# Optimization experiments

Hardware: AMD Instinct MI355X
Metric: run time of the kernel (lower is better)

## Reference

```python
import jax, jax.numpy as jnp
import numpy as np

HIDDEN = 2048
NUM_HEADS = 32
NUM_KV_HEADS = 8
HEAD_DIM = HIDDEN // NUM_HEADS  # 64


def setup_inputs() -> dict:
    key = jax.random.key(0)
    ks = jax.random.split(key, 5)
    s = 0.02
    x = jax.random.normal(ks[0], (2, 2048, HIDDEN), dtype=jnp.float32)
    Wq = jax.random.normal(ks[1], (HIDDEN, NUM_HEADS * HEAD_DIM), dtype=jnp.float32) * s
    Wk = jax.random.normal(ks[2], (HIDDEN, NUM_KV_HEADS * HEAD_DIM), dtype=jnp.float32) * s
    Wv = jax.random.normal(ks[3], (HIDDEN, NUM_KV_HEADS * HEAD_DIM), dtype=jnp.float32) * s
    Wo = jax.random.normal(ks[4], (NUM_HEADS * HEAD_DIM, HIDDEN), dtype=jnp.float32) * s
    return {"x": x, "Wq": Wq, "Wk": Wk, "Wv": Wv, "Wo": Wo}


def reference(x, Wq, Wk, Wv, Wo):
    b, s, _ = x.shape
    # projections: [b, s, h, d] -> [b, h, s, d]
    q = (x @ Wq).reshape(b, s, NUM_HEADS, HEAD_DIM).transpose(0, 2, 1, 3)
    k = (x @ Wk).reshape(b, s, NUM_KV_HEADS, HEAD_DIM).transpose(0, 2, 1, 3)
    v = (x @ Wv).reshape(b, s, NUM_KV_HEADS, HEAD_DIM).transpose(0, 2, 1, 3)
    rep = NUM_HEADS // NUM_KV_HEADS
    # repeat_interleave along head dim (consecutive copies), matching torch
    k = jnp.repeat(k, rep, axis=1)
    v = jnp.repeat(v, rep, axis=1)
    scale = HEAD_DIM ** (-0.5)
    attn = jnp.einsum("bhqd,bhkd->bhqk", q, k) * scale  # [b,h,s,s]
    attn = jax.nn.softmax(attn, axis=-1)
    out = jnp.einsum("bhqk,bhkd->bhqd", attn, v)
    out = out.transpose(0, 2, 1, 3).reshape(b, s, NUM_HEADS * HEAD_DIM)
    return out @ Wo
```

## Files before the change

### kernel.cpp

```cpp
#include <hip/hip_runtime.h>

typedef __attribute__((ext_vector_type(8))) short short8;
typedef __attribute__((ext_vector_type(4))) float f32x4;
typedef __attribute__((ext_vector_type(4))) unsigned short u16x4;
typedef __attribute__((ext_vector_type(8))) unsigned short u16x8;

__device__ __forceinline__ unsigned short f2bf(float f) {
  union { float f; unsigned u; } v; v.f = f;
  unsigned r = v.u + 0x7FFFu + ((v.u >> 16) & 1u);
  return (unsigned short)(r >> 16);
}

#define GLL16(g, l) \
  __builtin_amdgcn_global_load_lds((const __attribute__((address_space(1))) void*)(g), \
                                   (__attribute__((address_space(3))) void*)(l), 16, 0, 0)

__device__ __forceinline__ void tpose_body(const float* __restrict__ in,
                                           unsigned short* __restrict__ out,
                                           int C, int ldo, int c0, int r0,
                                           float (*tile)[33], int tx, int ty) {
#pragma unroll
  for (int i = 0; i < 4; ++i)
    tile[ty + i * 8][tx] = in[(size_t)(r0 + ty + i * 8) * C + c0 + tx];
  __syncthreads();
#pragma unroll
  for (int i = 0; i < 4; ++i)
    out[(size_t)(c0 + ty + i * 8) * ldo + r0 + tx] = f2bf(tile[tx][ty + i * 8]);
}

__global__ __launch_bounds__(256) void prep_kernel(const float* __restrict__ x,
                                                   const float* __restrict__ Wq,
                                                   const float* __restrict__ Wk,
                                                   const float* __restrict__ Wv,
                                                   const float* __restrict__ Wo,
                                                   unsigned short* __restrict__ xb,
                                                   unsigned short* __restrict__ wqkvt,
                                                   unsigned short* __restrict__ wot) {
  __shared__ float tile[32][33];
  const int bid = blockIdx.x;
  if (bid < 4096) {
    const int i = bid * 256 + threadIdx.x;
    const f32x4* p = (const f32x4*)x;
    f32x4 a = p[2 * i], b = p[2 * i + 1];
    u16x8 r;
    r[0] = f2bf(a[0]); r[1] = f2bf(a[1]); r[2] = f2bf(a[2]); r[3] = f2bf(a[3]);
    r[4] = f2bf(b[0]); r[5] = f2bf(b[1]); r[6] = f2bf(b[2]); r[7] = f2bf(b[3]);
    ((u16x8*)xb)[i] = r;
    return;
  }
  const int tx = threadIdx.x & 31, ty = threadIdx.x >> 5;
  int b2 = bid - 4096;
  if (b2 < 4096) {
    tpose_body(Wq, wqkvt, 2048, 2048, (b2 & 63) * 32, (b2 >> 6) * 32, tile, tx, ty);
    return;
  }
  b2 -= 4096;
  if (b2 < 1024) {
    tpose_body(Wk, wqkvt + (size_t)2048 * 2048, 512, 2048, (b2 & 15) * 32, (b2 >> 4) * 32, tile, tx, ty);
    return;
  }
  b2 -= 1024;
  if (b2 < 1024) {
    tpose_body(Wv, wqkvt + (size_t)2560 * 2048, 512, 2048, (b2 & 15) * 32, (b2 >> 4) * 32, tile, tx, ty);
    return;
  }
  b2 -= 1024;
  tpose_body(Wo, wot, 2048, 2048, (b2 & 63) * 32, (b2 >> 6) * 32, tile, tx, ty);
}

__global__ __launch_bounds__(256) void gemm_qkv_kernel(const unsigned short* __restrict__ A,
                                                       const unsigned short* __restrict__ BT,
                                                       unsigned short* __restrict__ Cq,
                                                       unsigned short* __restrict__ VT) {
  __shared__ unsigned short As[2][128 * 32];
  __shared__ unsigned short Bs[2][128 * 32];
  const int tid = threadIdx.x;
  const int wave = tid >> 6, lane = tid & 63;
  const int r16 = lane & 15, g = lane >> 4;
  const int n0 = blockIdx.x * 128, m0 = blockIdx.y * 128;
  const int wr = wave >> 1, wc = wave & 1;
  f32x4 acc[4][4] = {};
  const int so = wave * 1024 + lane * 16;

  auto STAGE = [&](int kt, int bufi) {
    const int k0 = kt * 32;
#pragma unroll
    for (int i = 0; i < 2; ++i) {
      const int o = i * 4096 + so;
      const int row = o >> 6;
      const int ke = (o & 63) >> 1;
      GLL16(A + (size_t)(m0 + row) * 2048 + k0 + ke, (char*)As[bufi] + i * 4096 + wave * 1024);
      GLL16(BT + (size_t)(n0 + row) * 2048 + k0 + ke, (char*)Bs[bufi] + i * 4096 + wave * 1024);
    }
  };
  STAGE(0, 0);
  __syncthreads();
  for (int kt = 0; kt < 64; ++kt) {
    const int cur = kt & 1;
    if (kt < 63) STAGE(kt + 1, cur ^ 1);
    short8 af[4], bfr[4];
#pragma unroll
    for (int mi = 0; mi < 4; ++mi) {
      const int row = wr * 64 + mi * 16 + r16;
      af[mi] = *(const short8*)((const char*)As[cur] + row * 64 + g * 16);
    }
#pragma unroll
    for (int ni = 0; ni < 4; ++ni) {
      const int row = wc * 64 + ni * 16 + r16;
      bfr[ni] = *(const short8*)((const char*)Bs[cur] + row * 64 + g * 16);
    }
#pragma unroll
    for (int mi = 0; mi < 4; ++mi)
#pragma unroll
      for (int ni = 0; ni < 4; ++ni)
        acc[mi][ni] = __builtin_amdgcn_mfma_f32_16x16x32_bf16(af[mi], bfr[ni], acc[mi][ni], 0, 0, 0);
    __syncthreads();
  }
  const float qs = 0.18033688f;
#pragma unroll
  for (int mi = 0; mi < 4; ++mi) {
#pragma unroll
    for (int ni = 0; ni < 4; ++ni) {
      const int n = n0 + wc * 64 + ni * 16 + r16;
      const int mb = m0 + wr * 64 + mi * 16 + g * 4;
      f32x4 v = acc[mi][ni];
      if (n < 2560) {
        const float s = (n < 2048) ? qs : 1.0f;
#pragma unroll
        for (int r = 0; r < 4; ++r) Cq[(size_t)(mb + r) * 3072 + n] = f2bf(v[r] * s);
      } else {
        const int d = n - 2560;
        const int bb = mb >> 11, s0 = mb & 2047;
        const int s0p = (s0 & ~31) | (((s0 >> 2) & 3) << 3) | (((s0 >> 4) & 1) << 2);
        u16x4 pk;
#pragma unroll
        for (int r = 0; r < 4; ++r) pk[r] = f2bf(v[r]);
        *(u16x4*)(VT + (size_t)(bb * 512 + d) * 2048 + s0p) = pk;
      }
    }
  }
}

__global__ __launch_bounds__(256) void gemm_out_kernel(const unsigned short* __restrict__ A,
                                                       const unsigned short* __restrict__ BT,
                                                       float* __restrict__ Co) {
  __shared__ unsigned short As[2][128 * 32];
  __shared__ unsigned short Bs[2][128 * 32];
  const int tid = threadIdx.x;
  const int wave = tid >> 6, lane = tid & 63;
  const int r16 = lane & 15, g = lane >> 4;
  const int n0 = blockIdx.x * 128, m0 = blockIdx.y * 128;
  const int wr = wave >> 1, wc = wave & 1;
  f32x4 acc[4][4] = {};
  const int so = wave * 1024 + lane * 16;

  auto STAGE = [&](int kt, int bufi) {
    const int k0 = kt * 32;
#pragma unroll
    for (int i = 0; i < 2; ++i) {
      const int o = i * 4096 + so;
      const int row = o >> 6;
      const int ke = (o & 63) >> 1;
      GLL16(A + (size_t)(m0 + row) * 2048 + k0 + ke, (char*)As[bufi] + i * 4096 + wave * 1024);
      GLL16(BT + (size_t)(n0 + row) * 2048 + k0 + ke, (char*)Bs[bufi] + i * 4096 + wave * 1024);
    }
  };
  STAGE(0, 0);
  __syncthreads();
  for (int kt = 0; kt < 64; ++kt) {
    const int cur = kt & 1;
    if (kt < 63) STAGE(kt + 1, cur ^ 1);
    short8 af[4], bfr[4];
#pragma unroll
    for (int mi = 0; mi < 4; ++mi) {
      const int row = wr * 64 + mi * 16 + r16;
      af[mi] = *(const short8*)((const char*)As[cur] + row * 64 + g * 16);
    }
#pragma unroll
    for (int ni = 0; ni < 4; ++ni) {
      const int row = wc * 64 + ni * 16 + r16;
      bfr[ni] = *(const short8*)((const char*)Bs[cur] + row * 64 + g * 16);
    }
#pragma unroll
    for (int mi = 0; mi < 4; ++mi)
#pragma unroll
      for (int ni = 0; ni < 4; ++ni)
        acc[mi][ni] = __builtin_amdgcn_mfma_f32_16x16x32_bf16(af[mi], bfr[ni], acc[mi][ni], 0, 0, 0);
    __syncthreads();
  }
#pragma unroll
  for (int mi = 0; mi < 4; ++mi)
#pragma unroll
    for (int ni = 0; ni < 4; ++ni) {
      const int n = n0 + wc * 64 + ni * 16 + r16;
      const int mb = m0 + wr * 64 + mi * 16 + g * 4;
      f32x4 v = acc[mi][ni];
#pragma unroll
      for (int r = 0; r < 4; ++r) Co[(size_t)(mb + r) * 2048 + n] = v[r];
    }
}

__global__ __launch_bounds__(256) void attn_kernel(const unsigned short* __restrict__ QKV,
                                                   const unsigned short* __restrict__ VT,
                                                   unsigned short* __restrict__ O) {
  __shared__ unsigned short Ks[2][64 * 64];
  __shared__ unsigned short Vs[2][64 * 64];
  const int tid = threadIdx.x;
  const int wave = tid >> 6, lane = tid & 63;
  const int r16 = lane & 15, g = lane >> 4;
  const int qt = blockIdx.x, bh = blockIdx.y;
  const int b = bh >> 5, h = bh & 31, kvh = h >> 2;
  const int qtok0 = b * 2048 + qt * 128 + wave * 32;
  short8 qf[2][2];
#pragma unroll
  for (int mt = 0; mt < 2; ++mt)
#pragma unroll
    for (int kh = 0; kh < 2; ++kh)
      qf[mt][kh] = *(const short8*)(QKV + (size_t)(qtok0 + mt * 16 + r16) * 3072 + h * 64 + kh * 32 + g * 8);
  union { unsigned u[4]; short8 s; } ones;
  ones.u[0] = ones.u[1] = ones.u[2] = ones.u[3] = 0x3F803F80u;
  f32x4 oa[2][4] = {};
  f32x4 lacc[2] = {};
  const unsigned short* Kb = QKV + (size_t)b * 2048 * 3072 + 2048 + kvh * 64;
  const unsigned short* Vb = VT + (size_t)(b * 512 + kvh * 64) * 2048;
  const int so = wave * 1024 + lane * 16;

  auto STAGE = [&](int t, int bufi) {
    const int kv0 = t * 64;
#pragma unroll
    for (int i = 0; i < 2; ++i) {
      const int o = i * 4096 + so;
      const int row = o >> 7;
      const int c = ((((o >> 4) & 7) ^ (row & 7))) * 8;
      GLL16(Kb + (size_t)(kv0 + row) * 3072 + c, (char*)Ks[bufi] + i * 4096 + wave * 1024);
      GLL16(Vb + (size_t)row * 2048 + kv0 + c, (char*)Vs[bufi] + i * 4096 + wave * 1024);
    }
  };
  STAGE(0, 0);
  __syncthreads();
  for (int t = 0; t < 32; ++t) {
    const int cur = t & 1;
    if (t < 31) STAGE(t + 1, cur ^ 1);
    f32x4 sc[2][4];
    __builtin_amdgcn_s_setprio(1);
#pragma unroll
    for (int jt = 0; jt < 4; ++jt) {
      short8 kf0, kf1;
      const int j = jt * 16 + r16;
      kf0 = *(const short8*)((const char*)Ks[cur] + j * 128 + ((g * 16) ^ ((j & 7) << 4)));
      kf1 = *(const short8*)((const char*)Ks[cur] + j * 128 + ((64 + g * 16) ^ ((j & 7) << 4)));
#pragma unroll
      for (int mt = 0; mt < 2; ++mt) {
        f32x4 z = {-8.f, -8.f, -8.f, -8.f};
        z = __builtin_amdgcn_mfma_f32_16x16x32_bf16(kf0, qf[mt][0], z, 0, 0, 0);
        z = __builtin_amdgcn_mfma_f32_16x16x32_bf16(kf1, qf[mt][1], z, 0, 0, 0);
        sc[mt][jt] = z;
      }
    }
    __builtin_amdgcn_s_setprio(0);
    short8 pa[2][2];
#pragma unroll
    for (int mt = 0; mt < 2; ++mt) {
      unsigned pk[4][2];
#pragma unroll
      for (int jt = 0; jt < 4; ++jt) {
        float p0 = __builtin_amdgcn_exp2f(sc[mt][jt][0]);
        float p1 = __builtin_amdgcn_exp2f(sc[mt][jt][1]);
        float p2 = __builtin_amdgcn_exp2f(sc[mt][jt][2]);
        float p3 = __builtin_amdgcn_exp2f(sc[mt][jt][3]);
        asm("v_cvt_pk_bf16_f32 %0, %1, %2" : "=v"(pk[jt][0]) : "v"(p0), "v"(p1));
        asm("v_cvt_pk_bf16_f32 %0, %1, %2" : "=v"(pk[jt][1]) : "v"(p2), "v"(p3));
      }
#pragma unroll
      for (int kh = 0; kh < 2; ++kh) {
        union { unsigned u[4]; short8 s; } pu;
        pu.u[0] = pk[2 * kh][0]; pu.u[1] = pk[2 * kh][1];
        pu.u[2] = pk[2 * kh + 1][0]; pu.u[3] = pk[2 * kh + 1][1];
        pa[mt][kh] = pu.s;
      }
    }
    __builtin_amdgcn_s_setprio(1);
#pragma unroll
    for (int mt = 0; mt < 2; ++mt) {
      lacc[mt] = __builtin_amdgcn_mfma_f32_16x16x32_bf16(pa[mt][0], ones.s, lacc[mt], 0, 0, 0);
      lacc[mt] = __builtin_amdgcn_mfma_f32_16x16x32_bf16(pa[mt][1], ones.s, lacc[mt], 0, 0, 0);
    }
#pragma unroll
    for (int dt = 0; dt < 4; ++dt) {
      const int d = dt * 16 + r16;
      const char* vrow = (const char*)Vs[cur] + d * 128;
      const int sw = (d & 7) << 4;
#pragma unroll
      for (int kh = 0; kh < 2; ++kh) {
        short8 vf = *(const short8*)(vrow + ((kh * 64 + g * 16) ^ sw));
#pragma unroll
        for (int mt = 0; mt < 2; ++mt)
          oa[mt][dt] = __builtin_amdgcn_mfma_f32_16x16x32_bf16(pa[mt][kh], vf, oa[mt][dt], 0, 0, 0);
      }
    }
    __builtin_amdgcn_s_setprio(0);
    __syncthreads();
  }
#pragma unroll
  for (int mt = 0; mt < 2; ++mt)
#pragma unroll
    for (int dt = 0; dt < 4; ++dt)
#pragma unroll
      for (int r = 0; r < 4; ++r)
        O[(size_t)(qtok0 + mt * 16 + g * 4 + r) * 2048 + h * 64 + dt * 16 + r16] =
            f2bf(oa[mt][dt][r] / lacc[mt][r]);
}

extern "C" void kernel_launch(void* const* d_in, const int* in_sizes, int n_in,
                              void* d_out, int out_size, void* d_ws, size_t ws_size,
                              hipStream_t stream) {
  const float* x  = (const float*)d_in[0];
  const float* Wq = (const float*)d_in[1];
  const float* Wk = (const float*)d_in[2];
  const float* Wv = (const float*)d_in[3];
  const float* Wo = (const float*)d_in[4];
  char* w = (char*)d_ws;
  unsigned short* xb    = (unsigned short*)(w);
  unsigned short* wqkvt = (unsigned short*)(w + 16777216);
  unsigned short* wot   = (unsigned short*)(w + 29360128);
  unsigned short* qkv   = (unsigned short*)(w + 37748736);
  unsigned short* vt    = (unsigned short*)(w + 62914560);
  unsigned short* ob    = (unsigned short*)(w + 67108864);
  float* out = (float*)d_out;

  prep_kernel<<<14336, 256, 0, stream>>>(x, Wq, Wk, Wv, Wo, xb, wqkvt, wot);
  gemm_qkv_kernel<<<dim3(24, 32), 256, 0, stream>>>(xb, wqkvt, qkv, vt);
  attn_kernel<<<dim3(16, 64), 256, 0, stream>>>(qkv, vt, ob);
  gemm_out_kernel<<<dim3(16, 32), 256, 0, stream>>>(ob, wot, out);
}
```

Before: 236.5 us.

## Split attention block into 8 waves of 16 query rows each

The attention kernel now launches 512 threads per block, and each of 8 waves handles 16 query rows instead of 32. The K/V staging is spread so each thread issues one global-to-LDS load per tile instead of two. This aims to raise wave-level parallelism and latency hiding per block while cutting per-wave registers. In exchange, each K/V fragment read from LDS now feeds only one query tile, so LDS read traffic per MFMA doubles, and the larger block synchronises more waves at each barrier.

```diff
diff --git a/kernel.cpp b/kernel.cpp
--- a/kernel.cpp
+++ b/kernel.cpp
@@ -200,7 +200,7 @@
     }
 }
 
-__global__ __launch_bounds__(256) void attn_kernel(const unsigned short* __restrict__ QKV,
+__global__ __launch_bounds__(512) void attn_kernel(const unsigned short* __restrict__ QKV,
                                                    const unsigned short* __restrict__ VT,
                                                    unsigned short* __restrict__ O) {
   __shared__ unsigned short Ks[2][64 * 64];
@@ -210,64 +210,53 @@
   const int r16 = lane & 15, g = lane >> 4;
   const int qt = blockIdx.x, bh = blockIdx.y;
   const int b = bh >> 5, h = bh & 31, kvh = h >> 2;
-  const int qtok0 = b * 2048 + qt * 128 + wave * 32;
-  short8 qf[2][2];
-#pragma unroll
-  for (int mt = 0; mt < 2; ++mt)
-#pragma unroll
-    for (int kh = 0; kh < 2; ++kh)
-      qf[mt][kh] = *(const short8*)(QKV + (size_t)(qtok0 + mt * 16 + r16) * 3072 + h * 64 + kh * 32 + g * 8);
+  const int qtok0 = b * 2048 + qt * 128 + wave * 16;
+  short8 qf[2];
+#pragma unroll
+  for (int kh = 0; kh < 2; ++kh)
+    qf[kh] = *(const short8*)(QKV + (size_t)(qtok0 + r16) * 3072 + h * 64 + kh * 32 + g * 8);
   union { unsigned u[4]; short8 s; } ones;
   ones.u[0] = ones.u[1] = ones.u[2] = ones.u[3] = 0x3F803F80u;
-  f32x4 oa[2][4] = {};
-  f32x4 lacc[2] = {};
+  f32x4 oa[4] = {};
+  f32x4 lacc = {};
   const unsigned short* Kb = QKV + (size_t)b * 2048 * 3072 + 2048 + kvh * 64;
   const unsigned short* Vb = VT + (size_t)(b * 512 + kvh * 64) * 2048;
   const int so = wave * 1024 + lane * 16;
 
   auto STAGE = [&](int t, int bufi) {
     const int kv0 = t * 64;
-#pragma unroll
-    for (int i = 0; i < 2; ++i) {
-      const int o = i * 4096 + so;
-      const int row = o >> 7;
-      const int c = ((((o >> 4) & 7) ^ (row & 7))) * 8;
-      GLL16(Kb + (size_t)(kv0 + row) * 3072 + c, (char*)Ks[bufi] + i * 4096 + wave * 1024);
-      GLL16(Vb + (size_t)row * 2048 + kv0 + c, (char*)Vs[bufi] + i * 4096 + wave * 1024);
-    }
+    const int row = so >> 7;
+    const int c = ((((so >> 4) & 7) ^ (row & 7))) * 8;
+    GLL16(Kb + (size_t)(kv0 + row) * 3072 + c, (char*)Ks[bufi] + wave * 1024);
+    GLL16(Vb + (size_t)row * 2048 + kv0 + c, (char*)Vs[bufi] + wave * 1024);
   };
   STAGE(0, 0);
   __syncthreads();
   for (int t = 0; t < 32; ++t) {
     const int cur = t & 1;
     if (t < 31) STAGE(t + 1, cur ^ 1);
-    f32x4 sc[2][4];
+    f32x4 sc[4];
     __builtin_amdgcn_s_setprio(1);
 #pragma unroll
     for (int jt = 0; jt < 4; ++jt) {
-      short8 kf0, kf1;
       const int j = jt * 16 + r16;
-      kf0 = *(const short8*)((const char*)Ks[cur] + j * 128 + ((g * 16) ^ ((j & 7) << 4)));
-      kf1 = *(const short8*)((const char*)Ks[cur] + j * 128 + ((64 + g * 16) ^ ((j & 7) << 4)));
-#pragma unroll
-      for (int mt = 0; mt < 2; ++mt) {
-        f32x4 z = {-8.f, -8.f, -8.f, -8.f};
-        z = __builtin_amdgcn_mfma_f32_16x16x32_bf16(kf0, qf[mt][0], z, 0, 0, 0);
-        z = __builtin_amdgcn_mfma_f32_16x16x32_bf16(kf1, qf[mt][1], z, 0, 0, 0);
-        sc[mt][jt] = z;
-      }
+      short8 kf0 = *(const short8*)((const char*)Ks[cur] + j * 128 + ((g * 16) ^ ((j & 7) << 4)));
+      short8 kf1 = *(const short8*)((const char*)Ks[cur] + j * 128 + ((64 + g * 16) ^ ((j & 7) << 4)));
+      f32x4 z = {-8.f, -8.f, -8.f, -8.f};
+      z = __builtin_amdgcn_mfma_f32_16x16x32_bf16(kf0, qf[0], z, 0, 0, 0);
+      z = __builtin_amdgcn_mfma_f32_16x16x32_bf16(kf1, qf[1], z, 0, 0, 0);
+      sc[jt] = z;
     }
     __builtin_amdgcn_s_setprio(0);
-    short8 pa[2][2];
-#pragma unroll
-    for (int mt = 0; mt < 2; ++mt) {
+    short8 pa[2];
+    {
       unsigned pk[4][2];
 #pragma unroll
       for (int jt = 0; jt < 4; ++jt) {
-        float p0 = __builtin_amdgcn_exp2f(sc[mt][jt][0]);
-        float p1 = __builtin_amdgcn_exp2f(sc[mt][jt][1]);
-        float p2 = __builtin_amdgcn_exp2f(sc[mt][jt][2]);
-        float p3 = __builtin_amdgcn_exp2f(sc[mt][jt][3]);
+        float p0 = __builtin_amdgcn_exp2f(sc[jt][0]);
+        float p1 = __builtin_amdgcn_exp2f(sc[jt][1]);
+        float p2 = __builtin_amdgcn_exp2f(sc[jt][2]);
+        float p3 = __builtin_amdgcn_exp2f(sc[jt][3]);
         asm("v_cvt_pk_bf16_f32 %0, %1, %2" : "=v"(pk[jt][0]) : "v"(p0), "v"(p1));
         asm("v_cvt_pk_bf16_f32 %0, %1, %2" : "=v"(pk[jt][1]) : "v"(p2), "v"(p3));
       }
@@ -276,15 +265,12 @@
         union { unsigned u[4]; short8 s; } pu;
         pu.u[0] = pk[2 * kh][0]; pu.u[1] = pk[2 * kh][1];
         pu.u[2] = pk[2 * kh + 1][0]; pu.u[3] = pk[2 * kh + 1][1];
-        pa[mt][kh] = pu.s;
+        pa[kh] = pu.s;
       }
     }
     __builtin_amdgcn_s_setprio(1);
-#pragma unroll
-    for (int mt = 0; mt < 2; ++mt) {
-      lacc[mt] = __builtin_amdgcn_mfma_f32_16x16x32_bf16(pa[mt][0], ones.s, lacc[mt], 0, 0, 0);
-      lacc[mt] = __builtin_amdgcn_mfma_f32_16x16x32_bf16(pa[mt][1], ones.s, lacc[mt], 0, 0, 0);
-    }
+    lacc = __builtin_amdgcn_mfma_f32_16x16x32_bf16(pa[0], ones.s, lacc, 0, 0, 0);
+    lacc = __builtin_amdgcn_mfma_f32_16x16x32_bf16(pa[1], ones.s, lacc, 0, 0, 0);
 #pragma unroll
     for (int dt = 0; dt < 4; ++dt) {
       const int d = dt * 16 + r16;
@@ -293,22 +279,18 @@
 #pragma unroll
       for (int kh = 0; kh < 2; ++kh) {
         short8 vf = *(const short8*)(vrow + ((kh * 64 + g * 16) ^ sw));
-#pragma unroll
-        for (int mt = 0; mt < 2; ++mt)
-          oa[mt][dt] = __builtin_amdgcn_mfma_f32_16x16x32_bf16(pa[mt][kh], vf, oa[mt][dt], 0, 0, 0);
+        oa[dt] = __builtin_amdgcn_mfma_f32_16x16x32_bf16(pa[kh], vf, oa[dt], 0, 0, 0);
       }
     }
     __builtin_amdgcn_s_setprio(0);
     __syncthreads();
   }
 #pragma unroll
-  for (int mt = 0; mt < 2; ++mt)
-#pragma unroll
-    for (int dt = 0; dt < 4; ++dt)
-#pragma unroll
-      for (int r = 0; r < 4; ++r)
-        O[(size_t)(qtok0 + mt * 16 + g * 4 + r) * 2048 + h * 64 + dt * 16 + r16] =
-            f2bf(oa[mt][dt][r] / lacc[mt][r]);
+  for (int dt = 0; dt < 4; ++dt)
+#pragma unroll
+    for (int r = 0; r < 4; ++r)
+      O[(size_t)(qtok0 + g * 4 + r) * 2048 + h * 64 + dt * 16 + r16] =
+          f2bf(oa[dt][r] / lacc[r]);
 }
 
 extern "C" void kernel_launch(void* const* d_in, const int* in_sizes, int n_in,
@@ -330,6 +312,6 @@
 
   prep_kernel<<<14336, 256, 0, stream>>>(x, Wq, Wk, Wv, Wo, xb, wqkvt, wot);
   gemm_qkv_kernel<<<dim3(24, 32), 256, 0, stream>>>(xb, wqkvt, qkv, vt);
-  attn_kernel<<<dim3(16, 64), 256, 0, stream>>>(qkv, vt, ob);
+  attn_kernel<<<dim3(16, 64), 512, 0, stream>>>(qkv, vt, ob);
   gemm_out_kernel<<<dim3(16, 32), 256, 0, stream>>>(ob, wot, out);
 }
```

Result: no change. 237.7 us (+0.5%).
